# Kernel optimization log

Hardware: AMD Instinct MI355X
Metric: run time of the kernel (lower is better)

Reference implementation:

```python
import jax, jax.numpy as jnp
import numpy as np

N_VAR = 100000
N_CON = 100000
N_EDGE = 2000000
C = 32  # all channel widths


def _linear(x, W, b):
    return x @ W.T + b


def setup_inputs() -> dict:
    key = jax.random.key(0)
    ks = jax.random.split(key, 16)
    s = 1.0 / np.sqrt(C)
    se = 1.0 / np.sqrt(3 * C)
    inp = {
        "var_f": jax.random.normal(ks[0], (N_VAR, C), jnp.float32),
        "con_f": jax.random.normal(ks[1], (N_CON, C), jnp.float32),
        "combined_edge_f": jax.random.normal(ks[2], (N_EDGE, C), jnp.float32),
        "edge_index_var_con": jax.random.randint(ks[3], (2, N_EDGE), 0, N_VAR, jnp.int32),
        # var_compress_mlp
        "Wv1": jax.random.uniform(ks[4], (C, C), jnp.float32, -s, s),
        "bv1": jnp.zeros((C,), jnp.float32),
        "Wv2": jax.random.uniform(ks[5], (C, C), jnp.float32, -s, s),
        "bv2": jnp.zeros((C,), jnp.float32),
        # con_compress_mlp
        "Wc1": jax.random.uniform(ks[6], (C, C), jnp.float32, -s, s),
        "bc1": jnp.zeros((C,), jnp.float32),
        "Wc2": jax.random.uniform(ks[7], (C, C), jnp.float32, -s, s),
        "bc2": jnp.zeros((C,), jnp.float32),
        # edge_mlp (input width = 3*C)
        "We1": jax.random.uniform(ks[8], (C, 3 * C), jnp.float32, -se, se),
        "be1": jnp.zeros((C,), jnp.float32),
        "We2": jax.random.uniform(ks[9], (C, C), jnp.float32, -s, s),
        "be2": jnp.zeros((C,), jnp.float32),
    }
    return inp


def reference(var_f, con_f, combined_edge_f, edge_index_var_con,
              Wv1, bv1, Wv2, bv2, Wc1, bc1, Wc2, bc2, We1, be1, We2, be2):
    # compress node features with 2-layer ReLU MLPs (done on nodes, not edges)
    v = jax.nn.relu(_linear(jax.nn.relu(_linear(var_f, Wv1, bv1)), Wv2, bv2))
    c = jax.nn.relu(_linear(jax.nn.relu(_linear(con_f, Wc1, bc1)), Wc2, bc2))
    # gather per-edge and concat: [E, 3C]
    out = jnp.concatenate(
        [combined_edge_f, v[edge_index_var_con[0]], c[edge_index_var_con[1]]], axis=1)
    # edge MLP: Linear -> ReLU -> Linear (no final ReLU)
    return _linear(jax.nn.relu(_linear(out, We1, be1)), We2, be2)
```

## Files before the change

### kernel.cpp

```cpp
#include <hip/hip_runtime.h>

typedef float  f32x2  __attribute__((ext_vector_type(2)));
typedef float  f32x4  __attribute__((ext_vector_type(4)));
typedef float  f32x16 __attribute__((ext_vector_type(16)));
typedef short  s16x4  __attribute__((ext_vector_type(4)));
typedef short  s16x8  __attribute__((ext_vector_type(8)));
typedef unsigned int u32x2 __attribute__((ext_vector_type(2)));

__device__ __forceinline__ unsigned f2bf(float f) {
    unsigned u = __builtin_bit_cast(unsigned, f);
    u += 0x7FFFu + ((u >> 16) & 1u);
    return u >> 16;
}
__device__ __forceinline__ s16x4 pack4(float a, float b, float c, float d) {
    u32x2 u;
    u[0] = f2bf(a) | (f2bf(b) << 16);
    u[1] = f2bf(c) | (f2bf(d) << 16);
    return __builtin_bit_cast(s16x4, u);
}
__device__ __forceinline__ s16x4 pack4v(f32x4 v) { return pack4(v[0], v[1], v[2], v[3]); }
__device__ __forceinline__ s16x4 lo4(s16x8 v) { return __builtin_shufflevector(v, v, 0, 1, 2, 3); }
__device__ __forceinline__ s16x4 hi4(s16x8 v) { return __builtin_shufflevector(v, v, 4, 5, 6, 7); }

__device__ __forceinline__ void node_body(
    const float* __restrict__ X,
    const float* __restrict__ W1, const float* __restrict__ b1,
    const float* __restrict__ W2, const float* __restrict__ b2,
    const float* __restrict__ Wm, const float* __restrict__ bm,
    unsigned short* __restrict__ outp, int N, int tile0)
{
    const int lane = threadIdx.x & 63;
    const int g = lane >> 5, m = lane & 31;
    const int ntile = (N + 31) >> 5;
    if (tile0 >= ntile) return;

    s16x4 a1[4], a2[4], am[4];
#pragma unroll
    for (int q = 0; q < 4; ++q) {
        const float* p1 = W1 + m * 32 + 8 * q + 4 * g;
        a1[q] = pack4(p1[0], p1[1], p1[2], p1[3]);
        const float* p2 = W2 + m * 32 + 8 * q + 4 * g;
        a2[q] = pack4(p2[0], p2[1], p2[2], p2[3]);
        const float* pm = Wm + m * 96 + 8 * q + 4 * g;
        am[q] = pack4(pm[0], pm[1], pm[2], pm[3]);
    }
    f32x16 f1, f2, f3;
#pragma unroll
    for (int r = 0; r < 16; ++r) {
        int ch = (r & 3) + 8 * (r >> 2) + 4 * g;
        f1[r] = b1[ch];
        f2[r] = b2[ch];
        f3[r] = bm ? bm[ch] : 0.f;
    }

#pragma unroll
    for (int k = 0; k < 4; ++k) {
        const int tile = tile0 + k;
        if (tile >= ntile) break;
        const int node0 = tile * 32 + m;
        const int node = node0 < N ? node0 : N - 1;

        s16x4 bX[4];
#pragma unroll
        for (int q = 0; q < 4; ++q) {
            f32x4 v = *reinterpret_cast<const f32x4*>(X + (size_t)node * 32 + 8 * q + 4 * g);
            bX[q] = pack4v(v);
        }
        f32x16 acc = f1;
#pragma unroll
        for (int q = 0; q < 4; ++q) acc = __builtin_amdgcn_mfma_f32_32x32x8bf16_1k(a1[q], bX[q], acc, 0, 0, 0);
        s16x4 bH[4];
#pragma unroll
        for (int q = 0; q < 4; ++q)
            bH[q] = pack4(fmaxf(acc[4*q+0], 0.f), fmaxf(acc[4*q+1], 0.f),
                          fmaxf(acc[4*q+2], 0.f), fmaxf(acc[4*q+3], 0.f));
        acc = f2;
#pragma unroll
        for (int q = 0; q < 4; ++q) acc = __builtin_amdgcn_mfma_f32_32x32x8bf16_1k(a2[q], bH[q], acc, 0, 0, 0);
#pragma unroll
        for (int q = 0; q < 4; ++q)
            bH[q] = pack4(fmaxf(acc[4*q+0], 0.f), fmaxf(acc[4*q+1], 0.f),
                          fmaxf(acc[4*q+2], 0.f), fmaxf(acc[4*q+3], 0.f));
        acc = f3;
#pragma unroll
        for (int q = 0; q < 4; ++q) acc = __builtin_amdgcn_mfma_f32_32x32x8bf16_1k(am[q], bH[q], acc, 0, 0, 0);

        if (node0 < N) {
#pragma unroll
            for (int q = 0; q < 4; ++q) {
                s16x4 o = pack4(acc[4*q+0], acc[4*q+1], acc[4*q+2], acc[4*q+3]);
                *reinterpret_cast<s16x4*>(outp + (size_t)node0 * 32 + 8 * q + 4 * g) = o;
            }
        }
    }
}

__global__ __launch_bounds__(256) void nodes_kernel(
    const float* __restrict__ var_f, const float* __restrict__ con_f,
    const float* __restrict__ Wv1, const float* __restrict__ bv1,
    const float* __restrict__ Wv2, const float* __restrict__ bv2,
    const float* __restrict__ Wc1, const float* __restrict__ bc1,
    const float* __restrict__ Wc2, const float* __restrict__ bc2,
    const float* __restrict__ We1, const float* __restrict__ be1,
    unsigned short* __restrict__ pv, unsigned short* __restrict__ pc,
    int nV, int nC, int wavesV)
{
    const int wvg = (blockIdx.x * blockDim.x + threadIdx.x) >> 6;
    if (wvg < wavesV) {
        node_body(var_f, Wv1, bv1, Wv2, bv2, We1 + 32, be1, pv, nV, wvg * 4);
    } else {
        node_body(con_f, Wc1, bc1, Wc2, bc2, We1 + 64, nullptr, pc, nC,
                  (wvg - wavesV) * 4);
    }
}

__global__ __launch_bounds__(256, 4) void edge_kernel(
    const float* __restrict__ Ef, const int* __restrict__ idx,
    const unsigned short* __restrict__ pv, const unsigned short* __restrict__ pc,
    const float* __restrict__ We1, const float* __restrict__ We2,
    const float* __restrict__ be2,
    float* __restrict__ out, int nE)
{
    __shared__ float ldso[4 * 1088];
    const int lane = threadIdx.x & 63;
    const int wv = threadIdx.x >> 6;
    const int g = lane >> 5, n = lane & 31;
    float* ldsw = ldso + wv * 1088;

    s16x4 aW1[4], aI[4], aW2[4];
#pragma unroll
    for (int q = 0; q < 4; ++q) {
        const float* p = We1 + n * 96 + 16 * g + 4 * q;
        aW1[q] = pack4(p[0], p[1], p[2], p[3]);
        s16x4 r;
#pragma unroll
        for (int j = 0; j < 4; ++j) r[j] = (short)((16 * g + 4 * q + j == n) ? 0x3F80 : 0);
        aI[q] = r;
        const float* p2 = We2 + n * 32 + 8 * q + 4 * g;
        aW2[q] = pack4(p2[0], p2[1], p2[2], p2[3]);
    }
    s16x4 aB2 = {}, bOne = {};
    if (g == 0) {
        aB2[0] = (short)f2bf(be2[n]);
        bOne[0] = (short)0x3F80;
    }

    const int ntile = nE >> 5;
    const int nw = (gridDim.x * blockDim.x) >> 6;
    int t = (blockIdx.x * blockDim.x + threadIdx.x) >> 6;
    if (t >= ntile) return;

    int e0 = t * 32 + n;
    int ia0 = idx[e0], ia1 = idx[nE + e0];
    const float* efp = Ef + (size_t)e0 * 32 + 16 * g;
    f32x4 ce0 = *reinterpret_cast<const f32x4*>(efp + 0);
    f32x4 ce1 = *reinterpret_cast<const f32x4*>(efp + 4);
    f32x4 ce2 = *reinterpret_cast<const f32x4*>(efp + 8);
    f32x4 ce3 = *reinterpret_cast<const f32x4*>(efp + 12);
    const unsigned short* pvr0 = pv + (size_t)ia0 * 32 + 16 * g;
    const unsigned short* pcr0 = pc + (size_t)ia1 * 32 + 16 * g;
    s16x8 cv0 = *reinterpret_cast<const s16x8*>(pvr0);
    s16x8 cv1 = *reinterpret_cast<const s16x8*>(pvr0 + 8);
    s16x8 cc0 = *reinterpret_cast<const s16x8*>(pcr0);
    s16x8 cc1 = *reinterpret_cast<const s16x8*>(pcr0 + 8);
    {
        int t1 = (t + nw < ntile) ? t + nw : t;
        int e1 = t1 * 32 + n;
        ia0 = idx[e1]; ia1 = idx[nE + e1];
    }
    int ib0 = ia0, ib1 = ia1;

    while (true) {
        const int tn = t + nw;
        const int tc = tn < ntile ? tn : t;

        const float* efpn = Ef + (size_t)(tc * 32 + n) * 32 + 16 * g;
        f32x4 ne0 = *reinterpret_cast<const f32x4*>(efpn + 0);
        f32x4 ne1 = *reinterpret_cast<const f32x4*>(efpn + 4);
        f32x4 ne2 = *reinterpret_cast<const f32x4*>(efpn + 8);
        f32x4 ne3 = *reinterpret_cast<const f32x4*>(efpn + 12);
        const unsigned short* pvn = pv + (size_t)ib0 * 32 + 16 * g;
        const unsigned short* pcn = pc + (size_t)ib1 * 32 + 16 * g;
        s16x8 nv0 = *reinterpret_cast<const s16x8*>(pvn);
        s16x8 nv1 = *reinterpret_cast<const s16x8*>(pvn + 8);
        s16x8 nc0 = *reinterpret_cast<const s16x8*>(pcn);
        s16x8 nc1 = *reinterpret_cast<const s16x8*>(pcn + 8);
        int t2 = (tn + nw < ntile) ? tn + nw : tc;
        int e2 = t2 * 32 + n;
        int ic0 = idx[e2], ic1 = idx[nE + e2];

        f32x16 acc = {};
        {
            s16x4 bE0 = pack4v(ce0), bE1 = pack4v(ce1), bE2 = pack4v(ce2), bE3 = pack4v(ce3);
            acc = __builtin_amdgcn_mfma_f32_32x32x8bf16_1k(aW1[0], bE0, acc, 0, 0, 0);
            acc = __builtin_amdgcn_mfma_f32_32x32x8bf16_1k(aW1[1], bE1, acc, 0, 0, 0);
            acc = __builtin_amdgcn_mfma_f32_32x32x8bf16_1k(aW1[2], bE2, acc, 0, 0, 0);
            acc = __builtin_amdgcn_mfma_f32_32x32x8bf16_1k(aW1[3], bE3, acc, 0, 0, 0);
        }
        acc = __builtin_amdgcn_mfma_f32_32x32x8bf16_1k(aI[0], lo4(cv0), acc, 0, 0, 0);
        acc = __builtin_amdgcn_mfma_f32_32x32x8bf16_1k(aI[1], hi4(cv0), acc, 0, 0, 0);
        acc = __builtin_amdgcn_mfma_f32_32x32x8bf16_1k(aI[2], lo4(cv1), acc, 0, 0, 0);
        acc = __builtin_amdgcn_mfma_f32_32x32x8bf16_1k(aI[3], hi4(cv1), acc, 0, 0, 0);
        acc = __builtin_amdgcn_mfma_f32_32x32x8bf16_1k(aI[0], lo4(cc0), acc, 0, 0, 0);
        acc = __builtin_amdgcn_mfma_f32_32x32x8bf16_1k(aI[1], hi4(cc0), acc, 0, 0, 0);
        acc = __builtin_amdgcn_mfma_f32_32x32x8bf16_1k(aI[2], lo4(cc1), acc, 0, 0, 0);
        acc = __builtin_amdgcn_mfma_f32_32x32x8bf16_1k(aI[3], hi4(cc1), acc, 0, 0, 0);

        s16x4 bH[4];
#pragma unroll
        for (int q = 0; q < 4; ++q)
            bH[q] = pack4(fmaxf(acc[4*q+0], 0.f), fmaxf(acc[4*q+1], 0.f),
                          fmaxf(acc[4*q+2], 0.f), fmaxf(acc[4*q+3], 0.f));

        f32x16 acc2 = {};
        acc2 = __builtin_amdgcn_mfma_f32_32x32x8bf16_1k(aB2, bOne, acc2, 0, 0, 0);
#pragma unroll
        for (int q = 0; q < 4; ++q)
            acc2 = __builtin_amdgcn_mfma_f32_32x32x8bf16_1k(aW2[q], bH[q], acc2, 0, 0, 0);

        {
            float* orow = ldsw + n * 34;
#pragma unroll
            for (int q = 0; q < 4; ++q) {
                f32x2 lo; lo[0] = acc2[4*q+0]; lo[1] = acc2[4*q+1];
                f32x2 hi; hi[0] = acc2[4*q+2]; hi[1] = acc2[4*q+3];
                *reinterpret_cast<f32x2*>(orow + 8 * q + 4 * g)     = lo;
                *reinterpret_cast<f32x2*>(orow + 8 * q + 4 * g + 2) = hi;
            }
            float* obase = out + (size_t)t * 1024;
#pragma unroll
            for (int p = 0; p < 4; ++p) {
                int li = p * 256 + lane * 4;
                int row = li >> 5, col = li & 31;
                const float* s = ldsw + row * 34 + col;
                f32x2 lo = *reinterpret_cast<const f32x2*>(s);
                f32x2 hi = *reinterpret_cast<const f32x2*>(s + 2);
                f32x4 v; v[0] = lo[0]; v[1] = lo[1]; v[2] = hi[0]; v[3] = hi[1];
                __builtin_nontemporal_store(v, reinterpret_cast<f32x4*>(obase + li));
            }
        }

        if (tn >= ntile) break;
        t = tn;
        ce0 = ne0; ce1 = ne1; ce2 = ne2; ce3 = ne3;
        cv0 = nv0; cv1 = nv1; cc0 = nc0; cc1 = nc1;
        ib0 = ic0; ib1 = ic1;
    }
}

extern "C" void kernel_launch(void* const* d_in, const int* in_sizes, int n_in,
                              void* d_out, int out_size, void* d_ws, size_t ws_size,
                              hipStream_t stream) {
    const float* var_f = (const float*)d_in[0];
    const float* con_f = (const float*)d_in[1];
    const float* Ef    = (const float*)d_in[2];
    const int*   idx   = (const int*)d_in[3];
    const float* Wv1 = (const float*)d_in[4];
    const float* bv1 = (const float*)d_in[5];
    const float* Wv2 = (const float*)d_in[6];
    const float* bv2 = (const float*)d_in[7];
    const float* Wc1 = (const float*)d_in[8];
    const float* bc1 = (const float*)d_in[9];
    const float* Wc2 = (const float*)d_in[10];
    const float* bc2 = (const float*)d_in[11];
    const float* We1 = (const float*)d_in[12];
    const float* be1 = (const float*)d_in[13];
    const float* We2 = (const float*)d_in[14];
    const float* be2 = (const float*)d_in[15];
    float* out = (float*)d_out;

    const int nV = in_sizes[0] / 32;
    const int nC = in_sizes[1] / 32;
    const int nE = in_sizes[2] / 32;

    unsigned short* pv = (unsigned short*)d_ws;
    unsigned short* pc = pv + (size_t)nV * 32;

    const int wavesV = (((nV + 31) >> 5) + 3) >> 2;
    const int wavesC = (((nC + 31) >> 5) + 3) >> 2;
    const int nodeBlocks = (wavesV + wavesC + 3) / 4;
    nodes_kernel<<<nodeBlocks, 256, 0, stream>>>(
        var_f, con_f, Wv1, bv1, Wv2, bv2, Wc1, bc1, Wc2, bc2,
        We1, be1, pv, pc, nV, nC, wavesV);

    edge_kernel<<<1024, 256, 0, stream>>>(Ef, idx, pv, pc, We1, We2, be2, out, nE);
}
```

Before: 169.9 us.

## Switch edge MLP from 32x32x8 to 16x16x16 bf16 MFMA tiles

Recasts the per-tile edge MLP as a 2x2 grid of 16x16x16 bf16 MFMAs in place of 32x32x8 MFMAs. The gathered node projections are still added through a permutation-matrix MFMA, and the second-layer bias now seeds the accumulator instead of costing an extra MFMA. The per-lane data layout changes so each lane loads 8 bf16 of each gathered row and 4 fp32 chunks of edge features. The bf16 packing of the prefetched edge features moves to the end of the loop. The aim is a cheaper MFMA instruction mix, at the cost of more instructions and a more complex register layout.

Measured after the change: 158.3 us, median of 2. 6.8% less time.

```diff
diff --git a/kernel.cpp b/kernel.cpp
--- a/kernel.cpp
+++ b/kernel.cpp
@@ -124,25 +124,29 @@
     __shared__ float ldso[4 * 1088];
     const int lane = threadIdx.x & 63;
     const int wv = threadIdx.x >> 6;
-    const int g = lane >> 5, n = lane & 31;
+    const int m = lane & 15, c = lane >> 4;
     float* ldsw = ldso + wv * 1088;
 
-    s16x4 aW1[4], aI[4], aW2[4];
-#pragma unroll
-    for (int q = 0; q < 4; ++q) {
-        const float* p = We1 + n * 96 + 16 * g + 4 * q;
-        aW1[q] = pack4(p[0], p[1], p[2], p[3]);
-        s16x4 r;
-#pragma unroll
-        for (int j = 0; j < 4; ++j) r[j] = (short)((16 * g + 4 * q + j == n) ? 0x3F80 : 0);
-        aI[q] = r;
-        const float* p2 = We2 + n * 32 + 8 * q + 4 * g;
-        aW2[q] = pack4(p2[0], p2[1], p2[2], p2[3]);
-    }
-    s16x4 aB2 = {}, bOne = {};
-    if (g == 0) {
-        aB2[0] = (short)f2bf(be2[n]);
-        bOne[0] = (short)0x3F80;
+    s16x4 aW1[2][2], aP[2][2], aW2[2][2];
+    f32x4 b2f[2];
+#pragma unroll
+    for (int r = 0; r < 2; ++r) {
+#pragma unroll
+        for (int kk = 0; kk < 2; ++kk) {
+            const float* p1 = We1 + (16 * r + m) * 96 + 16 * kk + 4 * c;
+            aW1[r][kk] = pack4(p1[0], p1[1], p1[2], p1[3]);
+            const float* p2 = We2 + (16 * r + m) * 32 + 16 * kk + 4 * c;
+            aW2[r][kk] = pack4(p2[0], p2[1], p2[2], p2[3]);
+            const int j_hit = 16 * r + m - 8 * c - 4 * kk;
+            s16x4 w;
+#pragma unroll
+            for (int j = 0; j < 4; ++j) w[j] = (short)((j == j_hit) ? 0x3F80 : 0);
+            aP[r][kk] = w;
+        }
+        f32x4 b;
+#pragma unroll
+        for (int j = 0; j < 4; ++j) b[j] = be2[16 * r + 4 * c + j];
+        b2f[r] = b;
     }
 
     const int ntile = nE >> 5;
@@ -150,89 +154,120 @@
     int t = (blockIdx.x * blockDim.x + threadIdx.x) >> 6;
     if (t >= ntile) return;
 
-    int e0 = t * 32 + n;
-    int ia0 = idx[e0], ia1 = idx[nE + e0];
-    const float* efp = Ef + (size_t)e0 * 32 + 16 * g;
-    f32x4 ce0 = *reinterpret_cast<const f32x4*>(efp + 0);
-    f32x4 ce1 = *reinterpret_cast<const f32x4*>(efp + 4);
-    f32x4 ce2 = *reinterpret_cast<const f32x4*>(efp + 8);
-    f32x4 ce3 = *reinterpret_cast<const f32x4*>(efp + 12);
-    const unsigned short* pvr0 = pv + (size_t)ia0 * 32 + 16 * g;
-    const unsigned short* pcr0 = pc + (size_t)ia1 * 32 + 16 * g;
-    s16x8 cv0 = *reinterpret_cast<const s16x8*>(pvr0);
-    s16x8 cv1 = *reinterpret_cast<const s16x8*>(pvr0 + 8);
-    s16x8 cc0 = *reinterpret_cast<const s16x8*>(pcr0);
-    s16x8 cc1 = *reinterpret_cast<const s16x8*>(pcr0 + 8);
+    int ib0[2], ib1[2];
+    s16x4 ebf[2][2];
+    s16x8 pvf[2], pcf[2];
     {
+        int i0[2], i1[2];
+#pragma unroll
+        for (int e = 0; e < 2; ++e) {
+            i0[e] = idx[t * 32 + 16 * e + m];
+            i1[e] = idx[nE + t * 32 + 16 * e + m];
+        }
+#pragma unroll
+        for (int e = 0; e < 2; ++e) {
+#pragma unroll
+            for (int kk = 0; kk < 2; ++kk) {
+                f32x4 v = *reinterpret_cast<const f32x4*>(
+                    Ef + (size_t)(t * 32 + 16 * e + m) * 32 + 16 * kk + 4 * c);
+                ebf[e][kk] = pack4v(v);
+            }
+            pvf[e] = *reinterpret_cast<const s16x8*>(pv + (size_t)i0[e] * 32 + 8 * c);
+            pcf[e] = *reinterpret_cast<const s16x8*>(pc + (size_t)i1[e] * 32 + 8 * c);
+        }
         int t1 = (t + nw < ntile) ? t + nw : t;
-        int e1 = t1 * 32 + n;
-        ia0 = idx[e1]; ia1 = idx[nE + e1];
-    }
-    int ib0 = ia0, ib1 = ia1;
+#pragma unroll
+        for (int e = 0; e < 2; ++e) {
+            ib0[e] = idx[t1 * 32 + 16 * e + m];
+            ib1[e] = idx[nE + t1 * 32 + 16 * e + m];
+        }
+    }
 
     while (true) {
         const int tn = t + nw;
         const int tc = tn < ntile ? tn : t;
 
-        const float* efpn = Ef + (size_t)(tc * 32 + n) * 32 + 16 * g;
-        f32x4 ne0 = *reinterpret_cast<const f32x4*>(efpn + 0);
-        f32x4 ne1 = *reinterpret_cast<const f32x4*>(efpn + 4);
-        f32x4 ne2 = *reinterpret_cast<const f32x4*>(efpn + 8);
-        f32x4 ne3 = *reinterpret_cast<const f32x4*>(efpn + 12);
-        const unsigned short* pvn = pv + (size_t)ib0 * 32 + 16 * g;
-        const unsigned short* pcn = pc + (size_t)ib1 * 32 + 16 * g;
-        s16x8 nv0 = *reinterpret_cast<const s16x8*>(pvn);
-        s16x8 nv1 = *reinterpret_cast<const s16x8*>(pvn + 8);
-        s16x8 nc0 = *reinterpret_cast<const s16x8*>(pcn);
-        s16x8 nc1 = *reinterpret_cast<const s16x8*>(pcn + 8);
-        int t2 = (tn + nw < ntile) ? tn + nw : tc;
-        int e2 = t2 * 32 + n;
-        int ic0 = idx[e2], ic1 = idx[nE + e2];
-
-        f32x16 acc = {};
+        f32x4 nef[2][2];
+        s16x8 npv[2], npc[2];
+        int ic0[2], ic1[2];
+#pragma unroll
+        for (int e = 0; e < 2; ++e) {
+#pragma unroll
+            for (int kk = 0; kk < 2; ++kk)
+                nef[e][kk] = *reinterpret_cast<const f32x4*>(
+                    Ef + (size_t)(tc * 32 + 16 * e + m) * 32 + 16 * kk + 4 * c);
+            npv[e] = *reinterpret_cast<const s16x8*>(pv + (size_t)ib0[e] * 32 + 8 * c);
+            npc[e] = *reinterpret_cast<const s16x8*>(pc + (size_t)ib1[e] * 32 + 8 * c);
+        }
         {
-            s16x4 bE0 = pack4v(ce0), bE1 = pack4v(ce1), bE2 = pack4v(ce2), bE3 = pack4v(ce3);
-            acc = __builtin_amdgcn_mfma_f32_32x32x8bf16_1k(aW1[0], bE0, acc, 0, 0, 0);
-            acc = __builtin_amdgcn_mfma_f32_32x32x8bf16_1k(aW1[1], bE1, acc, 0, 0, 0);
-            acc = __builtin_amdgcn_mfma_f32_32x32x8bf16_1k(aW1[2], bE2, acc, 0, 0, 0);
-            acc = __builtin_amdgcn_mfma_f32_32x32x8bf16_1k(aW1[3], bE3, acc, 0, 0, 0);
-        }
-        acc = __builtin_amdgcn_mfma_f32_32x32x8bf16_1k(aI[0], lo4(cv0), acc, 0, 0, 0);
-        acc = __builtin_amdgcn_mfma_f32_32x32x8bf16_1k(aI[1], hi4(cv0), acc, 0, 0, 0);
-        acc = __builtin_amdgcn_mfma_f32_32x32x8bf16_1k(aI[2], lo4(cv1), acc, 0, 0, 0);
-        acc = __builtin_amdgcn_mfma_f32_32x32x8bf16_1k(aI[3], hi4(cv1), acc, 0, 0, 0);
-        acc = __builtin_amdgcn_mfma_f32_32x32x8bf16_1k(aI[0], lo4(cc0), acc, 0, 0, 0);
-        acc = __builtin_amdgcn_mfma_f32_32x32x8bf16_1k(aI[1], hi4(cc0), acc, 0, 0, 0);
-        acc = __builtin_amdgcn_mfma_f32_32x32x8bf16_1k(aI[2], lo4(cc1), acc, 0, 0, 0);
-        acc = __builtin_amdgcn_mfma_f32_32x32x8bf16_1k(aI[3], hi4(cc1), acc, 0, 0, 0);
-
-        s16x4 bH[4];
-#pragma unroll
-        for (int q = 0; q < 4; ++q)
-            bH[q] = pack4(fmaxf(acc[4*q+0], 0.f), fmaxf(acc[4*q+1], 0.f),
-                          fmaxf(acc[4*q+2], 0.f), fmaxf(acc[4*q+3], 0.f));
-
-        f32x16 acc2 = {};
-        acc2 = __builtin_amdgcn_mfma_f32_32x32x8bf16_1k(aB2, bOne, acc2, 0, 0, 0);
-#pragma unroll
-        for (int q = 0; q < 4; ++q)
-            acc2 = __builtin_amdgcn_mfma_f32_32x32x8bf16_1k(aW2[q], bH[q], acc2, 0, 0, 0);
+            int t2 = (tn + nw < ntile) ? tn + nw : tc;
+#pragma unroll
+            for (int e = 0; e < 2; ++e) {
+                ic0[e] = idx[t2 * 32 + 16 * e + m];
+                ic1[e] = idx[nE + t2 * 32 + 16 * e + m];
+            }
+        }
+
+        f32x4 a00 = {}, a01 = {}, a10 = {}, a11 = {};
+        a00 = __builtin_amdgcn_mfma_f32_16x16x16bf16_1k(aW1[0][0], ebf[0][0], a00, 0, 0, 0);
+        a01 = __builtin_amdgcn_mfma_f32_16x16x16bf16_1k(aW1[0][0], ebf[1][0], a01, 0, 0, 0);
+        a10 = __builtin_amdgcn_mfma_f32_16x16x16bf16_1k(aW1[1][0], ebf[0][0], a10, 0, 0, 0);
+        a11 = __builtin_amdgcn_mfma_f32_16x16x16bf16_1k(aW1[1][0], ebf[1][0], a11, 0, 0, 0);
+        a00 = __builtin_amdgcn_mfma_f32_16x16x16bf16_1k(aW1[0][1], ebf[0][1], a00, 0, 0, 0);
+        a01 = __builtin_amdgcn_mfma_f32_16x16x16bf16_1k(aW1[0][1], ebf[1][1], a01, 0, 0, 0);
+        a10 = __builtin_amdgcn_mfma_f32_16x16x16bf16_1k(aW1[1][1], ebf[0][1], a10, 0, 0, 0);
+        a11 = __builtin_amdgcn_mfma_f32_16x16x16bf16_1k(aW1[1][1], ebf[1][1], a11, 0, 0, 0);
+        a00 = __builtin_amdgcn_mfma_f32_16x16x16bf16_1k(aP[0][0], lo4(pvf[0]), a00, 0, 0, 0);
+        a00 = __builtin_amdgcn_mfma_f32_16x16x16bf16_1k(aP[0][1], hi4(pvf[0]), a00, 0, 0, 0);
+        a01 = __builtin_amdgcn_mfma_f32_16x16x16bf16_1k(aP[0][0], lo4(pvf[1]), a01, 0, 0, 0);
+        a01 = __builtin_amdgcn_mfma_f32_16x16x16bf16_1k(aP[0][1], hi4(pvf[1]), a01, 0, 0, 0);
+        a10 = __builtin_amdgcn_mfma_f32_16x16x16bf16_1k(aP[1][0], lo4(pvf[0]), a10, 0, 0, 0);
+        a10 = __builtin_amdgcn_mfma_f32_16x16x16bf16_1k(aP[1][1], hi4(pvf[0]), a10, 0, 0, 0);
+        a11 = __builtin_amdgcn_mfma_f32_16x16x16bf16_1k(aP[1][0], lo4(pvf[1]), a11, 0, 0, 0);
+        a11 = __builtin_amdgcn_mfma_f32_16x16x16bf16_1k(aP[1][1], hi4(pvf[1]), a11, 0, 0, 0);
+        a00 = __builtin_amdgcn_mfma_f32_16x16x16bf16_1k(aP[0][0], lo4(pcf[0]), a00, 0, 0, 0);
+        a00 = __builtin_amdgcn_mfma_f32_16x16x16bf16_1k(aP[0][1], hi4(pcf[0]), a00, 0, 0, 0);
+        a01 = __builtin_amdgcn_mfma_f32_16x16x16bf16_1k(aP[0][0], lo4(pcf[1]), a01, 0, 0, 0);
+        a01 = __builtin_amdgcn_mfma_f32_16x16x16bf16_1k(aP[0][1], hi4(pcf[1]), a01, 0, 0, 0);
+        a10 = __builtin_amdgcn_mfma_f32_16x16x16bf16_1k(aP[1][0], lo4(pcf[0]), a10, 0, 0, 0);
+        a10 = __builtin_amdgcn_mfma_f32_16x16x16bf16_1k(aP[1][1], hi4(pcf[0]), a10, 0, 0, 0);
+        a11 = __builtin_amdgcn_mfma_f32_16x16x16bf16_1k(aP[1][0], lo4(pcf[1]), a11, 0, 0, 0);
+        a11 = __builtin_amdgcn_mfma_f32_16x16x16bf16_1k(aP[1][1], hi4(pcf[1]), a11, 0, 0, 0);
+
+        s16x4 bH00 = pack4(fmaxf(a00[0], 0.f), fmaxf(a00[1], 0.f), fmaxf(a00[2], 0.f), fmaxf(a00[3], 0.f));
+        s16x4 bH01 = pack4(fmaxf(a10[0], 0.f), fmaxf(a10[1], 0.f), fmaxf(a10[2], 0.f), fmaxf(a10[3], 0.f));
+        s16x4 bH10 = pack4(fmaxf(a01[0], 0.f), fmaxf(a01[1], 0.f), fmaxf(a01[2], 0.f), fmaxf(a01[3], 0.f));
+        s16x4 bH11 = pack4(fmaxf(a11[0], 0.f), fmaxf(a11[1], 0.f), fmaxf(a11[2], 0.f), fmaxf(a11[3], 0.f));
+
+        f32x4 o00 = b2f[0], o01 = b2f[0], o10 = b2f[1], o11 = b2f[1];
+        o00 = __builtin_amdgcn_mfma_f32_16x16x16bf16_1k(aW2[0][0], bH00, o00, 0, 0, 0);
+        o01 = __builtin_amdgcn_mfma_f32_16x16x16bf16_1k(aW2[0][0], bH10, o01, 0, 0, 0);
+        o10 = __builtin_amdgcn_mfma_f32_16x16x16bf16_1k(aW2[1][0], bH00, o10, 0, 0, 0);
+        o11 = __builtin_amdgcn_mfma_f32_16x16x16bf16_1k(aW2[1][0], bH10, o11, 0, 0, 0);
+        o00 = __builtin_amdgcn_mfma_f32_16x16x16bf16_1k(aW2[0][1], bH01, o00, 0, 0, 0);
+        o01 = __builtin_amdgcn_mfma_f32_16x16x16bf16_1k(aW2[0][1], bH11, o01, 0, 0, 0);
+        o10 = __builtin_amdgcn_mfma_f32_16x16x16bf16_1k(aW2[1][1], bH01, o10, 0, 0, 0);
+        o11 = __builtin_amdgcn_mfma_f32_16x16x16bf16_1k(aW2[1][1], bH11, o11, 0, 0, 0);
 
         {
-            float* orow = ldsw + n * 34;
-#pragma unroll
-            for (int q = 0; q < 4; ++q) {
-                f32x2 lo; lo[0] = acc2[4*q+0]; lo[1] = acc2[4*q+1];
-                f32x2 hi; hi[0] = acc2[4*q+2]; hi[1] = acc2[4*q+3];
-                *reinterpret_cast<f32x2*>(orow + 8 * q + 4 * g)     = lo;
-                *reinterpret_cast<f32x2*>(orow + 8 * q + 4 * g + 2) = hi;
+#pragma unroll
+            for (int r = 0; r < 2; ++r) {
+#pragma unroll
+                for (int e = 0; e < 2; ++e) {
+                    f32x4 o = (r == 0) ? (e == 0 ? o00 : o01) : (e == 0 ? o10 : o11);
+                    float* p = ldsw + (size_t)(16 * e + m) * 34 + 16 * r + 4 * c;
+                    f32x2 lo; lo[0] = o[0]; lo[1] = o[1];
+                    f32x2 hi; hi[0] = o[2]; hi[1] = o[3];
+                    *reinterpret_cast<f32x2*>(p)     = lo;
+                    *reinterpret_cast<f32x2*>(p + 2) = hi;
+                }
             }
             float* obase = out + (size_t)t * 1024;
 #pragma unroll
             for (int p = 0; p < 4; ++p) {
                 int li = p * 256 + lane * 4;
                 int row = li >> 5, col = li & 31;
-                const float* s = ldsw + row * 34 + col;
+                const float* s = ldsw + (size_t)row * 34 + col;
                 f32x2 lo = *reinterpret_cast<const f32x2*>(s);
                 f32x2 hi = *reinterpret_cast<const f32x2*>(s + 2);
                 f32x4 v; v[0] = lo[0]; v[1] = lo[1]; v[2] = hi[0]; v[3] = hi[1];
@@ -242,9 +277,13 @@
 
         if (tn >= ntile) break;
         t = tn;
-        ce0 = ne0; ce1 = ne1; ce2 = ne2; ce3 = ne3;
-        cv0 = nv0; cv1 = nv1; cc0 = nc0; cc1 = nc1;
-        ib0 = ic0; ib1 = ic1;
+#pragma unroll
+        for (int e = 0; e < 2; ++e) {
+#pragma unroll
+            for (int kk = 0; kk < 2; ++kk) ebf[e][kk] = pack4v(nef[e][kk]);
+            pvf[e] = npv[e]; pcf[e] = npc[e];
+            ib0[e] = ic0[e]; ib1[e] = ic1[e];
+        }
     }
 }
 
```
